# Optimization experiments

Measured on AMD Instinct MI355X. Metric: run time of the kernel, lower is better.

## Reference

```python
import math
import jax, jax.numpy as jnp
import numpy as np

_GELU_C = math.sqrt(2.0 / math.pi)

def _gelu_tanh(x):
    return 0.5 * x * (1.0 + jnp.tanh(_GELU_C * (x + 0.044715 * x * x * x)))

def _l2_normalize(v, eps=1e-12):
    # matches F.normalize: v / max(||v||, eps)
    n = jnp.sqrt(jnp.sum(v * v, axis=-1, keepdims=True))
    return v / jnp.maximum(n, eps)

def setup_inputs() -> dict:
    key = jax.random.key(0)
    k1, k2, k3 = jax.random.split(key, 3)
    B, T, D = 8, 2048, 1024
    x = jax.random.normal(k1, (B, T, D), dtype=jnp.float32)
    # nn.Parameter initial values from the module
    log_alpha = jnp.asarray(math.log(math.exp(0.5) - 1.0), dtype=jnp.float32)
    log_sigma = jnp.asarray(math.log(1.0), dtype=jnp.float32)
    return {"x": x, "log_alpha": log_alpha, "log_sigma": log_sigma}

def reference(x, log_alpha, log_sigma):
    B, T, D = x.shape
    alpha = jax.nn.softplus(log_alpha)
    sigma = jax.nn.softplus(log_sigma)
    scale = 1.0 / math.sqrt(D)
    # full strictly-past causal attention (triu with diagonal=0 masks self too)
    sim = jnp.einsum('btd,bsd->bts', x, x) * scale            # [B,T,T]
    causal = jnp.triu(jnp.ones((T, T), dtype=bool), k=0)      # True = masked
    sim = jnp.where(causal[None], -jnp.inf, sim)
    # NaN-safe masked softmax: fully-masked rows (t=0) -> all zeros,
    # matching torch softmax + nan_to_num(nan=0.0)
    m = jnp.max(sim, axis=-1, keepdims=True)
    m_safe = jnp.where(jnp.isfinite(m), m, 0.0)
    e = jnp.exp(sim - m_safe)                                 # -inf -> 0
    denom = jnp.sum(e, axis=-1, keepdims=True)
    attn = jnp.where(denom > 0, e / jnp.where(denom > 0, denom, 1.0), 0.0)
    context = jnp.einsum('bts,bsd->btd', attn, x)             # [B,T,D]
    cos_sim = jnp.sum(_l2_normalize(x) * _l2_normalize(context), axis=-1)  # [B,T]
    novelty = jnp.clip(1.0 - cos_sim, 0.0, 2.0) / 2.0
    novelty = jnp.nan_to_num(novelty, nan=1.0)
    gate = 1.0 + alpha * jnp.tanh(sigma * novelty[..., None])
    return _gelu_tanh(x * gate)
```

## Files before the change

kernel.cpp:

```cpp
#include <hip/hip_runtime.h>
#include <math.h>

#define TN 2048
#define DN 1024

typedef __attribute__((ext_vector_type(8))) _Float16 half8;
typedef __attribute__((ext_vector_type(4))) _Float16 half4v;
typedef __attribute__((ext_vector_type(4))) float f32x4;

__device__ __forceinline__ f32x4 mfma16(half8 a, half8 b, f32x4 c) {
  return __builtin_amdgcn_mfma_f32_16x16x32_f16(a, b, c, 0, 0, 0);
}

#define BAR_LDS()  asm volatile("s_waitcnt lgkmcnt(0)\ns_barrier" ::: "memory")
#define WAITVM0()  asm volatile("s_waitcnt vmcnt(0)" ::: "memory")

__device__ __forceinline__ int img_off(int key, int f) {
  const int kg = key >> 2;
  const int p  = ((kg & 1) << 2) | (kg >> 1);
  return (f >> 4) * 512 + p * 64 + (key & 3) * 16 + (f & 15);
}

__global__ __launch_bounds__(256) void convert_x(const float* __restrict__ x,
                                                 _Float16* __restrict__ w) {
  const long long gid = (long long)blockIdx.x * 256 + threadIdx.x;
  const long long e   = gid * 8;
  const int bt   = (int)(e >> 15);
  const int et   = (int)(e & 32767);
  const int f16b = et >> 9;
  const int p    = (et >> 6) & 7;
  const int row  = (et >> 4) & 3;
  const int col0 = et & 15;
  const int kg   = ((p & 3) << 1) | (p >> 2);
  const int key  = kg * 4 + row;
  const size_t xoff = ((size_t)bt * 32 + key) * DN + f16b * 16 + col0;
  float4 u0 = *(const float4*)(x + xoff);
  float4 u1 = *(const float4*)(x + xoff + 4);
  half8 h = {(_Float16)u0.x, (_Float16)u0.y, (_Float16)u0.z, (_Float16)u0.w,
             (_Float16)u1.x, (_Float16)u1.y, (_Float16)u1.z, (_Float16)u1.w};
  *(half8*)(w + e) = h;
}

#define ISSUE4(T, O0, O1, O2, O3)                                             \
  asm volatile("ds_read_b64_tr_b16 %0, %4 offset:" O0 "\n\t"                  \
               "ds_read_b64_tr_b16 %1, %4 offset:" O1 "\n\t"                  \
               "ds_read_b64_tr_b16 %2, %4 offset:" O2 "\n\t"                  \
               "ds_read_b64_tr_b16 %3, %4 offset:" O3                         \
               : "=&v"(T[0]), "=&v"(T[1]), "=&v"(T[2]), "=&v"(T[3])           \
               : "v"(ab));

#define MFMA2(T, CT0, CT1)                                                    \
  {                                                                           \
    half8 bf0 = __builtin_shufflevector(T[0], T[1], 0, 1, 2, 3, 4, 5, 6, 7);  \
    half8 bf1 = __builtin_shufflevector(T[2], T[3], 0, 1, 2, 3, 4, 5, 6, 7);  \
    oacc[CT0] = mfma16(aP, bf0, oacc[CT0]);                                   \
    oacc[CT1] = mfma16(aP, bf1, oacc[CT1]);                                   \
  }

template <bool WS>
__global__ __launch_bounds__(512, 4)
void attn_gate(const float* __restrict__ x, const _Float16* __restrict__ wsx,
               const float* __restrict__ pla, const float* __restrict__ pls,
               float* __restrict__ out) {
  __shared__ _Float16 Kbuf[32768];
  __shared__ _Float16 SredD[2][8][16][32];
  float* l_s    = (float*)&SredD[0][0][0][0];
  float* gate_s = l_s + 16;
  float* ered   = gate_s + 16;

  const int tid = threadIdx.x;
  const int w   = tid >> 6;
  const int l   = tid & 63;
  const int lr  = l & 15;
  const int lg  = l >> 4;
  const int kq  = w;

  const int b   = blockIdx.x & 7;
  const int q16 = 127 - (blockIdx.x >> 3);
  const int qbase = q16 * 16;
  const int nkt   = (qbase + 14) / 32 + 1;

  const float alpha = log1pf(expf(pla[0]));
  const float sigma = log1pf(expf(pls[0]));

  const float* xb = x + (size_t)b * TN * DN;
  float*       ob = out + (size_t)b * TN * DN;

  const int kg0 = lr >> 2;
  const int bk0 = ((((kg0 & 1) << 2) | (kg0 >> 1)) << 6) + (lr & 3) * 16 + (lg & 1) * 8;
  const int kg1 = 4 + (lr >> 2);
  const int bk1 = ((((kg1 & 1) << 2) | (kg1 >> 1)) << 6) + (lr & 3) * 16 + (lg & 1) * 8;

  const int swzA = (lg ^ (lr & 6)) << 2;
  const int swzB = ((4 + lg) ^ (lr & 6)) << 2;
  const int swzR = ((lg * 2) ^ (lr & 6)) << 2;

  auto STAGE = [&](int t) {
    if constexpr (WS) {
      const _Float16* tn = wsx + (size_t)(b * 64 + t) * 32768;
#pragma unroll
      for (int i = 0; i < 8; ++i)
        __builtin_amdgcn_global_load_lds(
            (const __attribute__((address_space(1))) void*)(tn + w * 4096 + i * 512 + l * 8),
            (__attribute__((address_space(3))) void*)(&Kbuf[w * 4096 + i * 512]), 16, 0, 0);
    } else {
      const int skey = tid >> 4, sc = tid & 15;
      const float* kp = xb + (size_t)(t * 32 + skey) * DN + sc * 4;
#pragma unroll
      for (int j = 0; j < 16; ++j) {
        const int f = sc * 4 + 64 * j;
        float4 v = *(const float4*)(kp + 64 * j);
        half4v h = {(_Float16)v.x, (_Float16)v.y, (_Float16)v.z, (_Float16)v.w};
        *(half4v*)&Kbuf[img_off(skey, f)] = h;
      }
    }
  };

  STAGE(0);

  half8 qf[4];
  if constexpr (WS) {
    const _Float16* qtile = wsx + (size_t)(b * 64 + (q16 >> 1)) * 32768;
    const int qrow = (q16 & 1) * 16 + lr;
    const int g0   = qrow >> 2;
    const int qp   = (((g0 & 1) << 2) | (g0 >> 1)) * 64 + (qrow & 3) * 16 + (lg & 1) * 8;
#pragma unroll
    for (int s = 0; s < 4; ++s)
      qf[s] = *(const half8*)&qtile[(kq * 8 + s * 2 + (lg >> 1)) * 512 + qp];
  } else {
#pragma unroll
    for (int s = 0; s < 4; ++s) {
      const float* qp = xb + (size_t)(qbase + lr) * DN + kq * 128 + s * 32 + lg * 8;
      float4 a = ((const float4*)qp)[0];
      float4 c = ((const float4*)qp)[1];
      half8 h;
      h[0]=(_Float16)a.x; h[1]=(_Float16)a.y; h[2]=(_Float16)a.z; h[3]=(_Float16)a.w;
      h[4]=(_Float16)c.x; h[5]=(_Float16)c.y; h[6]=(_Float16)c.z; h[7]=(_Float16)c.w;
      qf[s] = h;
    }
  }

  f32x4 oacc[8];
#pragma unroll
  for (int ct = 0; ct < 8; ++ct) oacc[ct] = f32x4{0.f, 0.f, 0.f, 0.f};
  float l0 = 0.0f;

  if constexpr (!WS) __syncthreads();

  for (int t = 0; t < nkt; ++t) {
    if constexpr (WS) WAITVM0();

    {
      f32x4 sA = f32x4{0.f,0.f,0.f,0.f};
      f32x4 sB = f32x4{0.f,0.f,0.f,0.f};
#pragma unroll
      for (int s = 0; s < 4; ++s) {
        const int base = (kq * 8 + s * 2 + (lg >> 1)) * 512;
        half8 bf0 = *(const half8*)&Kbuf[base + bk0];
        half8 bf1 = *(const half8*)&Kbuf[base + bk1];
        sA = mfma16(bf0, qf[s], sA);
        sB = mfma16(bf1, qf[s], sB);
      }
      half4v hA = {(_Float16)sA[0], (_Float16)sA[1], (_Float16)sA[2], (_Float16)sA[3]};
      half4v hB = {(_Float16)sB[0], (_Float16)sB[1], (_Float16)sB[2], (_Float16)sB[3]};
      _Float16* srow = &SredD[t & 1][kq][lr][0];
      *(half4v*)(srow + swzA) = hA;
      *(half4v*)(srow + swzB) = hB;
    }
    BAR_LDS();

    {
      const uint32_t ab = (uint32_t)(uintptr_t)(void*)&Kbuf[w * 4096 + l * 4];
      half4v t0[4], t1[4];
      ISSUE4(t0, "0", "512", "1024", "1536");
      ISSUE4(t1, "2048", "2560", "3072", "3584");

      const _Float16* sp = &SredD[t & 1][0][lr][0] + swzR;
      half8 sum = *(const half8*)(sp);
      sum = sum + *(const half8*)(sp + 512);
      sum = sum + *(const half8*)(sp + 1024);
      sum = sum + *(const half8*)(sp + 1536);
      sum = sum + *(const half8*)(sp + 2048);
      sum = sum + *(const half8*)(sp + 2560);
      sum = sum + *(const half8*)(sp + 3072);
      sum = sum + *(const half8*)(sp + 3584);

      const bool mt = (t == nkt - 1);
      const int  gb = 32 * t + lg * 8;
      half8 aP;
#pragma unroll
      for (int j = 0; j < 8; ++j) {
        float p = __expf((float)sum[j] * 0.03125f);
        if (mt && (gb + j >= qbase + lr)) p = 0.0f;
        l0 += p;
        aP[j] = (_Float16)p;
      }

      __builtin_amdgcn_sched_barrier(0);
      MFMA2(t0, 0, 1);
      ISSUE4(t0, "4096", "4608", "5120", "5632");
      asm volatile("s_waitcnt lgkmcnt(4)" ::: "memory");
      __builtin_amdgcn_sched_barrier(0);
      MFMA2(t1, 2, 3);
      ISSUE4(t1, "6144", "6656", "7168", "7680");
      asm volatile("s_waitcnt lgkmcnt(4)" ::: "memory");
      __builtin_amdgcn_sched_barrier(0);
      MFMA2(t0, 4, 5);
      asm volatile("s_waitcnt lgkmcnt(0)" ::: "memory");
      __builtin_amdgcn_sched_barrier(0);
      MFMA2(t1, 6, 7);
    }

    if (t + 1 < nkt) {
      if constexpr (!WS) __syncthreads();
      STAGE(t + 1);
      if constexpr (!WS) __syncthreads();
    }
  }

  BAR_LDS();

  {
    float lt = l0 + __shfl_xor(l0, 16);
    lt += __shfl_xor(lt, 32);
    if (w == 0 && lg == 0) l_s[lr] = lt;
  }

  {
#pragma unroll
    for (int j = 0; j < 4; ++j) {
      const int row = lg * 4 + j;
      const float* xr = xb + (size_t)(qbase + row) * DN + w * 128 + lr;
      float a1 = 0.f, a2 = 0.f, a3 = 0.f;
#pragma unroll
      for (int ct = 0; ct < 8; ++ct) {
        const float xv = xr[ct * 16];
        const float ov = oacc[ct][j];
        a1 += xv * ov; a2 += xv * xv; a3 += ov * ov;
      }
#pragma unroll
      for (int d = 1; d < 16; d <<= 1) {
        a1 += __shfl_xor(a1, d);
        a2 += __shfl_xor(a2, d);
        a3 += __shfl_xor(a3, d);
      }
      if (lr == 0) {
        float* e = ered + (row * 8 + w) * 4;
        e[0] = a1; e[1] = a2; e[2] = a3;
      }
    }
  }
  __syncthreads();
  if (tid < 16) {
    float SxO = 0.f, Sxx = 0.f, SOO = 0.f;
#pragma unroll
    for (int wv = 0; wv < 8; ++wv) {
      const float* e = ered + (tid * 8 + wv) * 4;
      SxO += e[0]; Sxx += e[1]; SOO += e[2];
    }
    const float lden = l_s[tid];
    float cosv = 0.0f;
    if (lden > 0.0f) {
      const float nx = fmaxf(sqrtf(Sxx), 1e-12f);
      const float nc = fmaxf(sqrtf(SOO) / lden, 1e-12f);
      cosv = (SxO / lden) / (nx * nc);
    }
    float nov = fminf(fmaxf(1.0f - cosv, 0.0f), 2.0f) * 0.5f;
    gate_s[tid] = 1.0f + alpha * tanhf(sigma * nov);
  }
  __syncthreads();
  {
#pragma unroll
    for (int j = 0; j < 4; ++j) {
      const int row = lg * 4 + j;
      const float g = gate_s[row];
      const float* xr = xb + (size_t)(qbase + row) * DN + w * 128 + lr;
      float* orow     = ob + (size_t)(qbase + row) * DN + w * 128 + lr;
#pragma unroll
      for (int ct = 0; ct < 8; ++ct) {
        const float z = xr[ct * 16] * g;
        const float u = 0.7978845608028654f * (z + 0.044715f * z * z * z);
        orow[ct * 16] = 0.5f * z * (1.0f + tanhf(u));
      }
    }
  }
}

extern "C" void kernel_launch(void* const* d_in, const int* in_sizes, int n_in,
                              void* d_out, int out_size, void* d_ws, size_t ws_size,
                              hipStream_t stream) {
  const float* x  = (const float*)d_in[0];
  const float* la = (const float*)d_in[1];
  const float* ls = (const float*)d_in[2];
  float* out = (float*)d_out;
  const size_t need = (size_t)8 * 64 * 32768 * 2;
  if (ws_size >= need) {
    convert_x<<<dim3(8192), dim3(256), 0, stream>>>(x, (_Float16*)d_ws);
    attn_gate<true><<<dim3(1024), dim3(512), 0, stream>>>(
        x, (const _Float16*)d_ws, la, ls, out);
  } else {
    attn_gate<false><<<dim3(1024), dim3(512), 0, stream>>>(
        x, (const _Float16*)nullptr, la, ls, out);
  }
}
```

Measured before the change: 187.2 us.

## Issue all V loads up front, move next-tile staging before PV MFMAs, use exp2

All 16 LDS reads of the value tile are now issued at once and waited on together. In the workspace path, the async load for the next key tile is issued before the PV MFMAs and exp, so that global load overlaps compute. The query fragments are pre-scaled by log2(e)/sqrt(D) so the softmax can use the hardware exp2 directly, packed fp16 conversion replaces scalar conversions, and the head-sum reduction becomes a tree. Costs are higher register pressure from holding 16 fragments, and slightly different fp16 rounding because the scale is applied to Q before the matmul.

```diff
diff --git a/kernel.cpp b/kernel.cpp
--- a/kernel.cpp
+++ b/kernel.cpp
@@ -6,6 +6,7 @@
 
 typedef __attribute__((ext_vector_type(8))) _Float16 half8;
 typedef __attribute__((ext_vector_type(4))) _Float16 half4v;
+typedef __attribute__((ext_vector_type(2))) _Float16 half2v;
 typedef __attribute__((ext_vector_type(4))) float f32x4;
 
 __device__ __forceinline__ f32x4 mfma16(half8 a, half8 b, f32x4 c) {
@@ -82,6 +83,7 @@
 
   const float alpha = log1pf(expf(pla[0]));
   const float sigma = log1pf(expf(pls[0]));
+  const float cs    = 0.0450842201f;
 
   const float* xb = x + (size_t)b * TN * DN;
   float*       ob = out + (size_t)b * TN * DN;
@@ -125,8 +127,12 @@
     const int g0   = qrow >> 2;
     const int qp   = (((g0 & 1) << 2) | (g0 >> 1)) * 64 + (qrow & 3) * 16 + (lg & 1) * 8;
 #pragma unroll
-    for (int s = 0; s < 4; ++s)
-      qf[s] = *(const half8*)&qtile[(kq * 8 + s * 2 + (lg >> 1)) * 512 + qp];
+    for (int s = 0; s < 4; ++s) {
+      half8 h = *(const half8*)&qtile[(kq * 8 + s * 2 + (lg >> 1)) * 512 + qp];
+#pragma unroll
+      for (int j = 0; j < 8; ++j) h[j] = (_Float16)((float)h[j] * cs);
+      qf[s] = h;
+    }
   } else {
 #pragma unroll
     for (int s = 0; s < 4; ++s) {
@@ -134,8 +140,10 @@
       float4 a = ((const float4*)qp)[0];
       float4 c = ((const float4*)qp)[1];
       half8 h;
-      h[0]=(_Float16)a.x; h[1]=(_Float16)a.y; h[2]=(_Float16)a.z; h[3]=(_Float16)a.w;
-      h[4]=(_Float16)c.x; h[5]=(_Float16)c.y; h[6]=(_Float16)c.z; h[7]=(_Float16)c.w;
+      h[0]=(_Float16)(a.x*cs); h[1]=(_Float16)(a.y*cs);
+      h[2]=(_Float16)(a.z*cs); h[3]=(_Float16)(a.w*cs);
+      h[4]=(_Float16)(c.x*cs); h[5]=(_Float16)(c.y*cs);
+      h[6]=(_Float16)(c.z*cs); h[7]=(_Float16)(c.w*cs);
       qf[s] = h;
     }
   }
@@ -171,50 +179,56 @@
 
     {
       const uint32_t ab = (uint32_t)(uintptr_t)(void*)&Kbuf[w * 4096 + l * 4];
-      half4v t0[4], t1[4];
+      half4v t0[4], t1[4], t2[4], t3[4];
       ISSUE4(t0, "0", "512", "1024", "1536");
       ISSUE4(t1, "2048", "2560", "3072", "3584");
+      ISSUE4(t2, "4096", "4608", "5120", "5632");
+      ISSUE4(t3, "6144", "6656", "7168", "7680");
 
       const _Float16* sp = &SredD[t & 1][0][lr][0] + swzR;
-      half8 sum = *(const half8*)(sp);
-      sum = sum + *(const half8*)(sp + 512);
-      sum = sum + *(const half8*)(sp + 1024);
-      sum = sum + *(const half8*)(sp + 1536);
-      sum = sum + *(const half8*)(sp + 2048);
-      sum = sum + *(const half8*)(sp + 2560);
-      sum = sum + *(const half8*)(sp + 3072);
-      sum = sum + *(const half8*)(sp + 3584);
+      half8 s0 = *(const half8*)(sp)        + *(const half8*)(sp + 512);
+      half8 s1 = *(const half8*)(sp + 1024) + *(const half8*)(sp + 1536);
+      half8 s2 = *(const half8*)(sp + 2048) + *(const half8*)(sp + 2560);
+      half8 s3 = *(const half8*)(sp + 3072) + *(const half8*)(sp + 3584);
+      half8 sum = (s0 + s1) + (s2 + s3);
+
+      asm volatile("s_waitcnt lgkmcnt(0)" ::: "memory");
+      __builtin_amdgcn_sched_barrier(0);
+
+      if constexpr (WS) {
+        if (t + 1 < nkt) STAGE(t + 1);
+      }
 
       const bool mt = (t == nkt - 1);
       const int  gb = 32 * t + lg * 8;
-      half8 aP;
-#pragma unroll
-      for (int j = 0; j < 8; ++j) {
-        float p = __expf((float)sum[j] * 0.03125f);
-        if (mt && (gb + j >= qbase + lr)) p = 0.0f;
-        l0 += p;
-        aP[j] = (_Float16)p;
-      }
+      union { uint32_t u[4]; half8 h; } ap;
+#pragma unroll
+      for (int k = 0; k < 4; ++k) {
+        float p0 = __builtin_amdgcn_exp2f((float)sum[2 * k]);
+        float p1 = __builtin_amdgcn_exp2f((float)sum[2 * k + 1]);
+        if (mt) {
+          if (gb + 2 * k     >= qbase + lr) p0 = 0.0f;
+          if (gb + 2 * k + 1 >= qbase + lr) p1 = 0.0f;
+        }
+        l0 += p0 + p1;
+        ap.u[k] = __builtin_bit_cast(uint32_t,
+                                     __builtin_amdgcn_cvt_pkrtz(p0, p1));
+      }
+      half8 aP = ap.h;
 
       __builtin_amdgcn_sched_barrier(0);
       MFMA2(t0, 0, 1);
-      ISSUE4(t0, "4096", "4608", "5120", "5632");
-      asm volatile("s_waitcnt lgkmcnt(4)" ::: "memory");
-      __builtin_amdgcn_sched_barrier(0);
       MFMA2(t1, 2, 3);
-      ISSUE4(t1, "6144", "6656", "7168", "7680");
-      asm volatile("s_waitcnt lgkmcnt(4)" ::: "memory");
-      __builtin_amdgcn_sched_barrier(0);
-      MFMA2(t0, 4, 5);
-      asm volatile("s_waitcnt lgkmcnt(0)" ::: "memory");
-      __builtin_amdgcn_sched_barrier(0);
-      MFMA2(t1, 6, 7);
-    }
-
-    if (t + 1 < nkt) {
-      if constexpr (!WS) __syncthreads();
-      STAGE(t + 1);
-      if constexpr (!WS) __syncthreads();
+      MFMA2(t2, 4, 5);
+      MFMA2(t3, 6, 7);
+    }
+
+    if constexpr (!WS) {
+      if (t + 1 < nkt) {
+        __syncthreads();
+        STAGE(t + 1);
+        __syncthreads();
+      }
     }
   }
 
```

Result: no change. 185.0 us (-1.2%).
